# Kernel tuning notes

Measured on AMD Instinct MI355X. Metric: run time of the kernel, lower is better.

## Reference

```python
import jax, jax.numpy as jnp
import numpy as np

L_MAX = 3
C = 512  # channels per degree


def _triples(l_max):
    ts = []
    for l1 in range(l_max + 1):
        for l2 in range(l1, l_max + 1):
            for L in range(l2 - l1, min(l_max, l1 + l2) + 1):
                ts.append((l1, l2, L))
    return ts


def setup_inputs() -> dict:
    key = jax.random.key(0)
    keys = jax.random.split(key, 4 + len(_triples(L_MAX)))
    inp = {}
    ki = 0
    for l in range(L_MAX + 1):
        inp[f"x{l}"] = jax.random.normal(keys[ki], (C, 2 * l + 1), dtype=jnp.float32)
        ki += 1
    for (l1, l2, L) in _triples(L_MAX):
        # cg[L, l2, l1] has shape [2L+1, 2l2+1, 2l1+1]
        inp[f"cg_{L}_{l2}_{l1}"] = 0.1 * jax.random.normal(
            keys[ki], (2 * L + 1, 2 * l2 + 1, 2 * l1 + 1), dtype=jnp.float32)
        ki += 1
    return inp


def reference(x0, x1, x2, x3,
              cg_0_0_0, cg_1_1_0, cg_2_2_0, cg_3_3_0,
              cg_0_1_1, cg_1_1_1, cg_2_1_1, cg_1_2_1, cg_2_2_1, cg_3_2_1,
              cg_2_3_1, cg_3_3_1,
              cg_0_2_2, cg_1_2_2, cg_2_2_2, cg_3_2_2, cg_1_3_2, cg_2_3_2,
              cg_3_3_2,
              cg_0_3_3, cg_1_3_3, cg_2_3_3, cg_3_3_3):
    xs = [x0, x1, x2, x3]
    cg_list = [cg_0_0_0, cg_1_1_0, cg_2_2_0, cg_3_3_0,
               cg_0_1_1, cg_1_1_1, cg_2_1_1, cg_1_2_1, cg_2_2_1, cg_3_2_1,
               cg_2_3_1, cg_3_3_1,
               cg_0_2_2, cg_1_2_2, cg_2_2_2, cg_3_2_2, cg_1_3_2, cg_2_3_2,
               cg_3_3_2,
               cg_0_3_3, cg_1_3_3, cg_2_3_3, cg_3_3_3]
    cg = dict(zip(_triples(L_MAX), cg_list))
    out = {L: [] for L in range(L_MAX + 1)}
    for (l1, l2, L) in _triples(L_MAX):
        # product: [i, j, 2L+1]
        p = jnp.einsum('Mnm,im,jn->ijM', cg[(l1, l2, L)], xs[l1], xs[l2])
        out[L].append(p.reshape(-1, 2 * L + 1))
    return tuple(jnp.concatenate(out[L], axis=0) for L in range(L_MAX + 1))
```

## Files before the change

### kernel.cpp

```cpp
#include <hip/hip_runtime.h>


#define CCH 512
#define C2 (512 * 512)

struct Ptrs {
    const float* x[4];
    const float* cg[23];
};

#define TRIPLE_LIST(F) \
    F(0, 0, 0, 0, 0, 0) \
    F(1, 0, 1, 1, 4, 1) \
    F(2, 0, 2, 2, 22, 10) \
    F(3, 0, 3, 3, 57, 35) \
    F(4, 1, 1, 0, 1, 84) \
    F(5, 1, 1, 1, 7, 87) \
    F(6, 1, 1, 2, 27, 96) \
    F(7, 1, 2, 1, 10, 111) \
    F(8, 1, 2, 2, 32, 126) \
    F(9, 1, 2, 3, 64, 151) \
    F(10, 1, 3, 2, 37, 186) \
    F(11, 1, 3, 3, 71, 221) \
    F(12, 2, 2, 0, 2, 270) \
    F(13, 2, 2, 1, 13, 275) \
    F(14, 2, 2, 2, 42, 290) \
    F(15, 2, 2, 3, 78, 315) \
    F(16, 2, 3, 1, 16, 350) \
    F(17, 2, 3, 2, 47, 371) \
    F(18, 2, 3, 3, 85, 406) \
    F(19, 3, 3, 0, 3, 455) \
    F(20, 3, 3, 1, 19, 462) \
    F(21, 3, 3, 2, 52, 483) \
    F(22, 3, 3, 3, 92, 518)

#define XBASE(L2) ((L2) == 0 ? 0 : ((L2) == 1 ? 1 : ((L2) == 2 ? 4 : 9)))

__global__ __launch_bounds__(256) void cg_tp_kernel(Ptrs p, float* __restrict__ out) {
    __shared__ float xT[16][256];
    __shared__ float ysh[567];

    const int tid = threadIdx.x;
    const int b = blockIdx.x;
    const int i = b >> 1;
    const int j0 = (b & 1) << 8;

    {
        const float* xp0 = p.x[0] + j0;
        xT[0][tid] = xp0[tid];

        const float* xp1 = p.x[1] + j0 * 3;
        #pragma unroll
        for (int r = 0; r < 3; ++r) {
            int idx = tid + r * 256;
            xT[1 + idx % 3][idx / 3] = xp1[idx];
        }
        const float* xp2 = p.x[2] + j0 * 5;
        #pragma unroll
        for (int r = 0; r < 5; ++r) {
            int idx = tid + r * 256;
            xT[4 + idx % 5][idx / 5] = xp2[idx];
        }
        const float* xp3 = p.x[3] + j0 * 7;
        #pragma unroll
        for (int r = 0; r < 7; ++r) {
            int idx = tid + r * 256;
            xT[9 + idx % 7][idx / 7] = xp3[idx];
        }
    }

    for (int e = tid; e < 567; e += 256) {
#define YC(T, L1, L2, LL, OB, YO)                                              \
        if (e >= (YO) && e < (YO) + (2 * L2 + 1) * (2 * LL + 1)) {             \
            const int local = e - (YO);                                        \
            const int n = local / (2 * LL + 1);                                \
            const int M = local % (2 * LL + 1);                                \
            const float* cg = p.cg[T] + (M * (2 * L2 + 1) + n) * (2 * L1 + 1); \
            const float* xi = p.x[L1] + i * (2 * L1 + 1);                      \
            float s = 0.f;                                                     \
            _Pragma("unroll")                                                  \
            for (int m = 0; m < 2 * L1 + 1; ++m) s = fmaf(cg[m], xi[m], s);    \
            ysh[e] = s;                                                        \
        }
        TRIPLE_LIST(YC)
#undef YC
    }

    __syncthreads();

    float xj[16];
    #pragma unroll
    for (int k = 0; k < 16; ++k) xj[k] = xT[k][tid];

    const int pair = b * 256 + tid;

#define TC(T, L1, L2, LL, OB, YO)                                              \
    {                                                                          \
        constexpr int NW = 2 * LL + 1;                                         \
        float acc[NW] = {};                                                    \
        const float* y = ysh + (YO);                                           \
        _Pragma("unroll")                                                      \
        for (int n = 0; n < 2 * L2 + 1; ++n) {                                 \
            const float xv = xj[XBASE(L2) + n];                                \
            _Pragma("unroll")                                                  \
            for (int M = 0; M < NW; ++M)                                       \
                acc[M] = fmaf(y[n * NW + M], xv, acc[M]);                      \
        }                                                                      \
        float* o = out + (size_t)(OB) * C2 + (size_t)pair * NW;                \
        _Pragma("unroll")                                                      \
        for (int M = 0; M < NW; ++M) o[M] = acc[M];                            \
    }
    TRIPLE_LIST(TC)
#undef TC
}

extern "C" void kernel_launch(void* const* d_in, const int* in_sizes, int n_in,
                              void* d_out, int out_size, void* d_ws, size_t ws_size,
                              hipStream_t stream) {
    Ptrs p;
    for (int l = 0; l < 4; ++l) p.x[l] = (const float*)d_in[l];
    for (int t = 0; t < 23; ++t) p.cg[t] = (const float*)d_in[4 + t];
    cg_tp_kernel<<<dim3(1024), dim3(256), 0, stream>>>(p, (float*)d_out);
}
```

Measured before the change: 172.6 us.

## Split triples across two block halves, drop xT staging, pad y rows

Doubles the grid so each block handles only half of the 23 triples for a given (i, j-half), spreading the output writes across more blocks. The x_j values are now loaded directly from global memory into registers instead of being staged through a transposed shared buffer. The y table is laid out with rows padded to 8 floats, and each row-thread computes all M entries. This is meant to raise parallelism and cut LDS staging. The cost is that y is computed twice per pair of blocks and the x loads become strided per-thread global loads.

```diff
diff --git a/kernel.cpp b/kernel.cpp
--- a/kernel.cpp
+++ b/kernel.cpp
@@ -1,7 +1,6 @@
 #include <hip/hip_runtime.h>
 
 
-#define CCH 512
 #define C2 (512 * 512)
 
 struct Ptrs {
@@ -10,101 +9,92 @@
 };
 
 #define TRIPLE_LIST(F) \
-    F(0, 0, 0, 0, 0, 0) \
-    F(1, 0, 1, 1, 4, 1) \
-    F(2, 0, 2, 2, 22, 10) \
-    F(3, 0, 3, 3, 57, 35) \
-    F(4, 1, 1, 0, 1, 84) \
-    F(5, 1, 1, 1, 7, 87) \
-    F(6, 1, 1, 2, 27, 96) \
-    F(7, 1, 2, 1, 10, 111) \
-    F(8, 1, 2, 2, 32, 126) \
-    F(9, 1, 2, 3, 64, 151) \
-    F(10, 1, 3, 2, 37, 186) \
-    F(11, 1, 3, 3, 71, 221) \
-    F(12, 2, 2, 0, 2, 270) \
-    F(13, 2, 2, 1, 13, 275) \
-    F(14, 2, 2, 2, 42, 290) \
-    F(15, 2, 2, 3, 78, 315) \
-    F(16, 2, 3, 1, 16, 350) \
-    F(17, 2, 3, 2, 47, 371) \
-    F(18, 2, 3, 3, 85, 406) \
-    F(19, 3, 3, 0, 3, 455) \
-    F(20, 3, 3, 1, 19, 462) \
-    F(21, 3, 3, 2, 52, 483) \
-    F(22, 3, 3, 3, 92, 518)
+    F(0, 0, 0, 0, 0, 0, 0) \
+    F(1, 0, 1, 1, 4, 1, 0) \
+    F(2, 0, 2, 2, 22, 4, 1) \
+    F(3, 0, 3, 3, 57, 9, 0) \
+    F(4, 1, 1, 0, 1, 16, 0) \
+    F(5, 1, 1, 1, 7, 19, 1) \
+    F(6, 1, 1, 2, 27, 22, 1) \
+    F(7, 1, 2, 1, 10, 25, 1) \
+    F(8, 1, 2, 2, 32, 30, 1) \
+    F(9, 1, 2, 3, 64, 35, 0) \
+    F(10, 1, 3, 2, 37, 40, 1) \
+    F(11, 1, 3, 3, 71, 47, 0) \
+    F(12, 2, 2, 0, 2, 54, 0) \
+    F(13, 2, 2, 1, 13, 59, 1) \
+    F(14, 2, 2, 2, 42, 64, 1) \
+    F(15, 2, 2, 3, 78, 69, 0) \
+    F(16, 2, 3, 1, 16, 74, 1) \
+    F(17, 2, 3, 2, 47, 81, 1) \
+    F(18, 2, 3, 3, 85, 88, 0) \
+    F(19, 3, 3, 0, 3, 95, 0) \
+    F(20, 3, 3, 1, 19, 102, 1) \
+    F(21, 3, 3, 2, 52, 109, 1) \
+    F(22, 3, 3, 3, 92, 116, 0)
 
 #define XBASE(L2) ((L2) == 0 ? 0 : ((L2) == 1 ? 1 : ((L2) == 2 ? 4 : 9)))
 
 __global__ __launch_bounds__(256) void cg_tp_kernel(Ptrs p, float* __restrict__ out) {
-    __shared__ float xT[16][256];
-    __shared__ float ysh[567];
+    __shared__ float ysh[123 * 8];
 
     const int tid = threadIdx.x;
     const int b = blockIdx.x;
-    const int i = b >> 1;
-    const int j0 = (b & 1) << 8;
+    const int i = b >> 2;
+    const int jh = (b >> 1) & 1;
+    const int half = b & 1;
+    const int j = (jh << 8) + tid;
 
-    {
-        const float* xp0 = p.x[0] + j0;
-        xT[0][tid] = xp0[tid];
-
-        const float* xp1 = p.x[1] + j0 * 3;
-        #pragma unroll
-        for (int r = 0; r < 3; ++r) {
-            int idx = tid + r * 256;
-            xT[1 + idx % 3][idx / 3] = xp1[idx];
-        }
-        const float* xp2 = p.x[2] + j0 * 5;
-        #pragma unroll
-        for (int r = 0; r < 5; ++r) {
-            int idx = tid + r * 256;
-            xT[4 + idx % 5][idx / 5] = xp2[idx];
-        }
-        const float* xp3 = p.x[3] + j0 * 7;
-        #pragma unroll
-        for (int r = 0; r < 7; ++r) {
-            int idx = tid + r * 256;
-            xT[9 + idx % 7][idx / 7] = xp3[idx];
-        }
-    }
-
-    for (int e = tid; e < 567; e += 256) {
-#define YC(T, L1, L2, LL, OB, YO)                                              \
-        if (e >= (YO) && e < (YO) + (2 * L2 + 1) * (2 * LL + 1)) {             \
-            const int local = e - (YO);                                        \
-            const int n = local / (2 * LL + 1);                                \
-            const int M = local % (2 * LL + 1);                                \
-            const float* cg = p.cg[T] + (M * (2 * L2 + 1) + n) * (2 * L1 + 1); \
+    if (tid < 123) {
+        const int r = tid;
+#define YC(T, L1, L2, LL, OB, RB, HF)                                          \
+        if (r >= (RB) && r < (RB) + (2 * L2 + 1)) {                            \
+            const int n = r - (RB);                                            \
+            const float* cg = p.cg[T];                                         \
             const float* xi = p.x[L1] + i * (2 * L1 + 1);                      \
-            float s = 0.f;                                                     \
             _Pragma("unroll")                                                  \
-            for (int m = 0; m < 2 * L1 + 1; ++m) s = fmaf(cg[m], xi[m], s);    \
-            ysh[e] = s;                                                        \
+            for (int M = 0; M < 2 * LL + 1; ++M) {                             \
+                float s = 0.f;                                                 \
+                _Pragma("unroll")                                              \
+                for (int m = 0; m < 2 * L1 + 1; ++m)                           \
+                    s = fmaf(cg[(M * (2 * L2 + 1) + n) * (2 * L1 + 1) + m],    \
+                             xi[m], s);                                        \
+                ysh[r * 8 + M] = s;                                            \
+            }                                                                  \
         }
         TRIPLE_LIST(YC)
 #undef YC
     }
 
+    float xj[16];
+    {
+        xj[0] = p.x[0][j];
+        const float* x1 = p.x[1] + j * 3;
+        #pragma unroll
+        for (int m = 0; m < 3; ++m) xj[1 + m] = x1[m];
+        const float* x2 = p.x[2] + j * 5;
+        #pragma unroll
+        for (int m = 0; m < 5; ++m) xj[4 + m] = x2[m];
+        const float* x3 = p.x[3] + j * 7;
+        #pragma unroll
+        for (int m = 0; m < 7; ++m) xj[9 + m] = x3[m];
+    }
+
     __syncthreads();
 
-    float xj[16];
-    #pragma unroll
-    for (int k = 0; k < 16; ++k) xj[k] = xT[k][tid];
+    const int pair = i * 512 + j;
 
-    const int pair = b * 256 + tid;
-
-#define TC(T, L1, L2, LL, OB, YO)                                              \
-    {                                                                          \
+#define TC(T, L1, L2, LL, OB, RB, HF)                                          \
+    if (half == (HF)) {                                                        \
         constexpr int NW = 2 * LL + 1;                                         \
         float acc[NW] = {};                                                    \
-        const float* y = ysh + (YO);                                           \
+        const float* y = ysh + (RB) * 8;                                       \
         _Pragma("unroll")                                                      \
         for (int n = 0; n < 2 * L2 + 1; ++n) {                                 \
             const float xv = xj[XBASE(L2) + n];                                \
             _Pragma("unroll")                                                  \
             for (int M = 0; M < NW; ++M)                                       \
-                acc[M] = fmaf(y[n * NW + M], xv, acc[M]);                      \
+                acc[M] = fmaf(y[n * 8 + M], xv, acc[M]);                       \
         }                                                                      \
         float* o = out + (size_t)(OB) * C2 + (size_t)pair * NW;                \
         _Pragma("unroll")                                                      \
@@ -120,5 +110,5 @@
     Ptrs p;
     for (int l = 0; l < 4; ++l) p.x[l] = (const float*)d_in[l];
     for (int t = 0; t < 23; ++t) p.cg[t] = (const float*)d_in[4 + t];
-    cg_tp_kernel<<<dim3(1024), dim3(256), 0, stream>>>(p, (float*)d_out);
+    cg_tp_kernel<<<dim3(2048), dim3(256), 0, stream>>>(p, (float*)d_out);
 }
```

New measurement: 176.5 us. 1.02x slower.
